# Performance work log

Hardware: AMD Instinct MI355X
Metric: run time of the kernel (lower is better)

## Reference

```python
import jax, jax.numpy as jnp
import numpy as np

N_V = 6890  # SMPL vertices
N_J = 24    # SMPL joints
# standard SMPL kinematic tree: PARENT[i-1] is parent of joint i (i=1..23)
PARENT = np.array([0, 0, 0, 1, 2, 3, 4, 5, 6, 7, 8, 9, 9, 9, 12, 13, 14, 16, 17, 18, 19, 20, 21], dtype=np.int64)


def rodrigues(r):
    """Axis-angle [N,3] -> rotation matrices [N,3,3] (batch Rodrigues)."""
    angle = jnp.sqrt(jnp.sum(r * r, axis=-1, keepdims=True) + 1e-8)  # [N,1]
    axis = r / angle
    c = jnp.cos(angle)[..., None]  # [N,1,1]
    s = jnp.sin(angle)[..., None]
    x, y, z = axis[..., 0], axis[..., 1], axis[..., 2]
    zeros = jnp.zeros_like(x)
    K = jnp.stack([zeros, -z, y, z, zeros, -x, -y, x, zeros], axis=-1).reshape(-1, 3, 3)
    outer = axis[..., :, None] * axis[..., None, :]
    I = jnp.eye(3, dtype=r.dtype)
    return c * I + (1.0 - c) * outer + s * K


def setup_inputs() -> dict:
    key = jax.random.key(0)
    ks = jax.random.split(key, 7)
    B = 1024
    pose = jax.random.normal(ks[0], (B, 72), dtype=jnp.float32) * 0.4
    beta = jax.random.normal(ks[1], (B, 10), dtype=jnp.float32)
    shapedirs = jax.random.normal(ks[2], (N_V, 3, 10), dtype=jnp.float32) * 0.03
    posedirs = jax.random.normal(ks[3], (N_V, 3, 207), dtype=jnp.float32) * 0.01
    v_template = jax.random.normal(ks[4], (N_V, 3), dtype=jnp.float32)
    Jreg = jax.random.uniform(ks[5], (N_J, N_V), dtype=jnp.float32)
    J_regressor = Jreg / jnp.sum(Jreg, axis=1, keepdims=True)  # rows sum to 1 like SMPL
    w = jax.random.uniform(ks[6], (N_V, N_J), dtype=jnp.float32)
    weights = w / jnp.sum(w, axis=1, keepdims=True)  # convex skinning weights
    return {"pose": pose, "beta": beta, "shapedirs": shapedirs, "posedirs": posedirs,
            "v_template": v_template, "J_regressor": J_regressor, "weights": weights}


def reference(pose, beta, shapedirs, posedirs, v_template, J_regressor, weights):
    B = pose.shape[0]
    # shape blend shapes: v_shaped = shapedirs @ beta + template  [B,6890,3]
    v_shaped = jnp.einsum('vcs,bs->bvc', shapedirs, beta) + v_template[None]
    J = jnp.einsum('jv,bvc->bjc', J_regressor, v_shaped)
    # pose -> rotation matrices
    R = rodrigues(pose.reshape(-1, 3)).reshape(B, N_J, 3, 3)
    # pose blend shapes from (R - I) of non-root joints  [B,207]
    lrotmin = (R[:, 1:] - jnp.eye(3, dtype=R.dtype)).reshape(B, 207)
    v_posed = v_shaped + jnp.einsum('vcp,bp->bvc', posedirs, lrotmin)
    # relative joint locations
    J_rel = jnp.concatenate([J[:, :1], J[:, 1:] - J[:, PARENT]], axis=1)  # [B,24,3]
    # local transforms [B,24,4,4]
    G_top = jnp.concatenate([R, J_rel[..., None]], axis=-1)  # [B,24,3,4]
    pad_row = jnp.broadcast_to(jnp.array([0., 0., 0., 1.], dtype=R.dtype), (B, N_J, 1, 4))
    G_local = jnp.concatenate([G_top, pad_row], axis=2)
    # forward kinematics along the chain (fixed 24-joint loop)
    Gs = [G_local[:, 0]]
    for i in range(1, N_J):
        Gs.append(jnp.matmul(Gs[PARENT[i - 1]], G_local[:, i]))
    G = jnp.stack(Gs, axis=1)  # [B,24,4,4]
    # remove rest-pose transform: subtract G @ [J,0] from last column
    J_h = jnp.concatenate([J, jnp.zeros((B, N_J, 1), dtype=J.dtype)], axis=2)  # [B,24,4]
    corr = jnp.einsum('bjmn,bjn->bjm', G, J_h)  # [B,24,4]
    G = G - jnp.pad(corr[..., None], ((0, 0), (0, 0), (0, 0), (3, 0)))
    # skinning: per-vertex transform T = weights @ G  [B,6890,4,4]
    T = jnp.einsum('vj,bjmn->bvmn', weights, G)
    v_h = jnp.concatenate([v_posed, jnp.ones((B, N_V, 1), dtype=v_posed.dtype)], axis=-1)
    v = jnp.einsum('bvmn,bvn->bvm', T, v_h)[..., :3]
    return v
```

## Files before the change

### kernel.cpp

```cpp
#include <hip/hip_runtime.h>
#include <hip/hip_bf16.h>

#define N_V 6890
#define NVPAD 6912
#define N_J 24
#define NREAL 20670
#define NPROWS 27648
#define KDIM 224
#define FB 64
#define FV 64
#define SHP 260
#define NXT 108

typedef __attribute__((ext_vector_type(8))) short bf16x8;
typedef __attribute__((ext_vector_type(4))) float f32x4;

__constant__ int c_par[23] = {0,0,0,1,2,3,4,5,6,7,8,9,9,9,12,13,14,16,17,18,19,20,21};

static __device__ __forceinline__ unsigned short f2bf(float f) {
    unsigned int u = __float_as_uint(f);
    unsigned int r = (u + 0x7fffu + ((u >> 16) & 1u)) >> 16;
    return (unsigned short)r;
}
static __device__ __forceinline__ unsigned int pkbf(float a, float b) {
    return ((__float_as_uint(a) + 0x8000u) >> 16) |
           ((__float_as_uint(b) + 0x8000u) & 0xffff0000u);
}
static __device__ __forceinline__ size_t fragidx(int r, int k) {
    return ((size_t)((r >> 4) * 7 + (k >> 5)) << 9) +
           ((size_t)((r & 15) + (((k >> 3) & 3) << 4)) << 3) + (k & 7);
}

#define WS_PARTIAL 0
#define WS_USHORT  7128
#define U_AMF  0
#define U_BPF  229376
#define U_GBF  6422528
#define U_WBF  6946816

#define JREG_BLOCKS 192
#define BPF_BLOCKS  (NPROWS / 16)
#define WBF_BLOCKS  (NVPAD * 32 / 256)

static __device__ __forceinline__ float bval(const float* pd, const float* sd,
                                             const float* vt, int nc, int k) {
    if (k < 207)  return pd[(size_t)nc * 207 + k];
    if (k < 217)  return sd[(size_t)nc * 10 + (k - 207)];
    if (k == 217) return vt[nc];
    return 0.f;
}

__global__ __launch_bounds__(256)
void k_pre(const float* __restrict__ Jreg,
           const float* __restrict__ shapedirs,
           const float* __restrict__ v_template,
           const float* __restrict__ posedirs,
           const float* __restrict__ weights,
           float* __restrict__ partial,
           unsigned short* __restrict__ Bpf,
           unsigned short* __restrict__ Wbf) {
    const int bid = blockIdx.x;
    const int tid = threadIdx.x;

    if (bid < JREG_BLOCKS) {
        const int j = bid >> 3, chunk = bid & 7;
        const int per = (N_V + 7) / 8;
        const int v0 = chunk * per;
        const int v1 = (v0 + per < N_V) ? (v0 + per) : N_V;
        float acc[33];
#pragma unroll
        for (int k = 0; k < 33; ++k) acc[k] = 0.f;
        for (int v = v0 + tid; v < v1; v += 256) {
            const float w = Jreg[j * N_V + v];
            const float* sd = shapedirs + (size_t)v * 30;
#pragma unroll
            for (int k = 0; k < 30; ++k) acc[k] += w * sd[k];
            acc[30] += w * v_template[v * 3 + 0];
            acc[31] += w * v_template[v * 3 + 1];
            acc[32] += w * v_template[v * 3 + 2];
        }
#pragma unroll
        for (int k = 0; k < 33; ++k) {
            float x = acc[k];
            for (int off = 32; off > 0; off >>= 1) x += __shfl_down(x, off);
            acc[k] = x;
        }
        __shared__ float red[4][33];
        const int wave = tid >> 6, lane = tid & 63;
        if (lane == 0) {
#pragma unroll
            for (int k = 0; k < 33; ++k) red[wave][k] = acc[k];
        }
        __syncthreads();
        if (tid < 33) {
            partial[(j * 8 + chunk) * 33 + tid] =
                red[0][tid] + red[1][tid] + red[2][tid] + red[3][tid];
        }
    } else if (bid < JREG_BLOCKS + BPF_BLOCKS) {
        __shared__ float tile[16][228];
        const int r16 = bid - JREG_BLOCKS;
        {
            const int row = tid >> 4;
            const int k0 = (tid & 15) * 14;
            const int np = r16 * 16 + row;
            const int v = np >> 2, cc = np & 3;
            if (cc < 3 && v < N_V) {
                const int nc = v * 3 + cc;
                const float* pd = posedirs + (size_t)nc * 207;
#pragma unroll
                for (int i = 0; i < 14; ++i) {
                    const int k = k0 + i;
                    float val;
                    if (k < 207)       val = pd[k];
                    else if (k < 217)  val = shapedirs[(size_t)nc * 10 + (k - 207)];
                    else if (k == 217) val = v_template[nc];
                    else               val = 0.f;
                    tile[row][k] = val;
                }
            } else {
#pragma unroll
                for (int i = 0; i < 14; ++i) tile[row][k0 + i] = 0.f;
            }
        }
        __syncthreads();
        const int l = tid >> 2;
        const int row = l & 15;
        const int kblk = (l >> 4) * 8;
        const int e2 = (tid & 3) * 2;
        unsigned short* dst = Bpf + ((size_t)r16 * 7) * 512 + (size_t)tid * 2;
#pragma unroll
        for (int ks = 0; ks < 7; ++ks) {
            const int k = ks * 32 + kblk + e2;
            ushort2 o;
            o.x = f2bf(tile[row][k]);
            o.y = f2bf(tile[row][k + 1]);
            *(ushort2*)(dst + (size_t)ks * 512) = o;
        }
    } else {
        const int idx = (bid - JREG_BLOCKS - BPF_BLOCKS) * 256 + tid;
        const int v = idx >> 5, k = idx & 31;
        float val = (v < N_V && k < 24) ? weights[(size_t)v * 24 + k] : 0.f;
        Wbf[idx] = f2bf(val);
    }
}

__global__ __launch_bounds__(512)
void k_joints(const float* __restrict__ pose, const float* __restrict__ beta,
              const float* __restrict__ partial,
              unsigned short* __restrict__ Amf,
              unsigned short* __restrict__ Gbf) {
    const int tid = threadIdx.x;
    const int wid = tid >> 6;
    const int j = tid & 63;
    const int b = blockIdx.x * 8 + wid;
    __shared__ float sJS[24][30];
    __shared__ float sJt_[24][3];
    __shared__ float sJ[8][24][3];
    __shared__ float sG[8][24][12];

    for (int idx = tid; idx < 792; idx += 512) {
        const int jj = idx / 33, kk = idx - jj * 33;
        float s = 0.f;
#pragma unroll
        for (int c = 0; c < 8; ++c) s += partial[(jj * 8 + c) * 33 + kk];
        if (kk < 30) sJS[jj][kk] = s;
        else         sJt_[jj][kk - 30] = s;
    }

    for (int idx = j; idx < 224; idx += 64) {
        int mn, jj;
        if (idx < 128) { mn = 12 + (idx >> 5); jj = idx & 31; }
        else { const int q = idx - 128; mn = q >> 3; jj = 24 + (q & 7); }
        Gbf[(size_t)b * 512 + mn * 32 + jj] = 0;
    }
    __syncthreads();

    float R[9];
    if (j < 24) {
        const float* bt = beta + b * 10;
#pragma unroll
        for (int c = 0; c < 3; ++c) {
            float s = sJt_[j][c];
#pragma unroll
            for (int t = 0; t < 10; ++t) s += sJS[j][c * 10 + t] * bt[t];
            sJ[wid][j][c] = s;
        }
        const float rx = pose[b * 72 + 3 * j + 0];
        const float ry = pose[b * 72 + 3 * j + 1];
        const float rz = pose[b * 72 + 3 * j + 2];
        const float ang = sqrtf(rx * rx + ry * ry + rz * rz + 1e-8f);
        const float inv = 1.f / ang;
        const float x = rx * inv, y = ry * inv, z = rz * inv;
        const float c = cosf(ang), s = sinf(ang);
        const float ic = 1.f - c;
        R[0] = c + ic * x * x;     R[1] = ic * x * y - s * z; R[2] = ic * x * z + s * y;
        R[3] = ic * x * y + s * z; R[4] = c + ic * y * y;     R[5] = ic * y * z - s * x;
        R[6] = ic * x * z - s * y; R[7] = ic * y * z + s * x; R[8] = c + ic * z * z;
        if (j >= 1) {
            const int kb = (j - 1) * 9;
#pragma unroll
            for (int k = 0; k < 9; ++k)
                Amf[fragidx(b & 15, kb + k) + (size_t)(b >> 4) * 3584] =
                    f2bf(R[k] - ((k == 0 || k == 4 || k == 8) ? 1.f : 0.f));
        }
    } else if (j < 41) {
        const int k = 207 + (j - 24);
        float val = (k < 217) ? beta[b * 10 + (k - 207)] : (k == 217 ? 1.f : 0.f);
        Amf[fragidx(b & 15, k) + (size_t)(b >> 4) * 3584] = f2bf(val);
    }
    __syncthreads();
    if (j < 24) {
        float t0, t1, t2;
        if (j == 0) { t0 = sJ[wid][0][0]; t1 = sJ[wid][0][1]; t2 = sJ[wid][0][2]; }
        else {
            const int p = c_par[j - 1];
            t0 = sJ[wid][j][0] - sJ[wid][p][0];
            t1 = sJ[wid][j][1] - sJ[wid][p][1];
            t2 = sJ[wid][j][2] - sJ[wid][p][2];
        }
        sG[wid][j][0] = R[0]; sG[wid][j][1] = R[1]; sG[wid][j][2]  = R[2]; sG[wid][j][3]  = t0;
        sG[wid][j][4] = R[3]; sG[wid][j][5] = R[4]; sG[wid][j][6]  = R[5]; sG[wid][j][7]  = t1;
        sG[wid][j][8] = R[6]; sG[wid][j][9] = R[7]; sG[wid][j][10] = R[8]; sG[wid][j][11] = t2;
    }
    __syncthreads();
    if (j == 0) {
        for (int i = 1; i < 24; ++i) {
            const int p = c_par[i - 1];
            float P[12], L[12];
#pragma unroll
            for (int k = 0; k < 12; ++k) { P[k] = sG[wid][p][k]; L[k] = sG[wid][i][k]; }
#pragma unroll
            for (int m = 0; m < 3; ++m) {
#pragma unroll
                for (int n = 0; n < 3; ++n)
                    sG[wid][i][m * 4 + n] = P[m * 4] * L[n] + P[m * 4 + 1] * L[4 + n] + P[m * 4 + 2] * L[8 + n];
                sG[wid][i][m * 4 + 3] = P[m * 4] * L[3] + P[m * 4 + 1] * L[7] + P[m * 4 + 2] * L[11] + P[m * 4 + 3];
            }
        }
    }
    __syncthreads();
    if (j < 24) {
        const float jx = sJ[wid][j][0], jy = sJ[wid][j][1], jz = sJ[wid][j][2];
#pragma unroll
        for (int m = 0; m < 3; ++m) {
            const float corr = sG[wid][j][m * 4] * jx + sG[wid][j][m * 4 + 1] * jy + sG[wid][j][m * 4 + 2] * jz;
            Gbf[(size_t)b * 512 + (m * 4 + 0) * 32 + j] = f2bf(sG[wid][j][m * 4 + 0]);
            Gbf[(size_t)b * 512 + (m * 4 + 1) * 32 + j] = f2bf(sG[wid][j][m * 4 + 1]);
            Gbf[(size_t)b * 512 + (m * 4 + 2) * 32 + j] = f2bf(sG[wid][j][m * 4 + 2]);
            Gbf[(size_t)b * 512 + (m * 4 + 3) * 32 + j] = f2bf(sG[wid][j][m * 4 + 3] - corr);
        }
    }
}

__global__ __launch_bounds__(512, 4)
void k_fused(const unsigned short* __restrict__ Amf,
             const unsigned short* __restrict__ Bpf,
             const unsigned short* __restrict__ Gbf,
             const unsigned short* __restrict__ Wbf,
             float* __restrict__ out) {
    __shared__ unsigned short sH[FB * SHP];
    const int tid = threadIdx.x;
    const int wid = tid >> 6, l = tid & 63;
    const int c16 = l & 15, p = l >> 4;

    const int wg = ((blockIdx.x & 7) * 216) + (blockIdx.x >> 3);
    const int xt = wg >> 4;
    const int bg = wg & 15;
    const int v0 = xt * FV;
    const int b0 = bg * FB;

    bf16x8 bw[4];
#pragma unroll
    for (int g = 0; g < 4; ++g)
        bw[g] = *(const bf16x8*)&Wbf[(size_t)(v0 + g * 16 + c16) * 32 + p * 8];
    const int bwv = wid * 8;
    const unsigned short* gG = Gbf + (size_t)(b0 + bwv) * 512 + c16 * 32 + p * 8;

    f32x4 acc[2][4];
#pragma unroll
    for (int i = 0; i < 2; ++i)
#pragma unroll
        for (int j = 0; j < 4; ++j) acc[i][j] = (f32x4){0.f, 0.f, 0.f, 0.f};

    const unsigned short* pbf = Bpf + ((size_t)(xt * 16 + wid * 2) * 7) * 512 + (size_t)l * 8;
    const unsigned short* pam = Amf + ((size_t)(bg * 4) * 7) * 512 + (size_t)l * 8;

#pragma unroll
    for (int ks = 0; ks < 7; ++ks) {
        bf16x8 af[2], bfr[4];
#pragma unroll
        for (int mi = 0; mi < 2; ++mi)
            af[mi] = *(const bf16x8*)(pbf + (size_t)(mi * 7 + ks) * 512);
#pragma unroll
        for (int bj = 0; bj < 4; ++bj)
            bfr[bj] = *(const bf16x8*)(pam + (size_t)(bj * 7 + ks) * 512);
        __builtin_amdgcn_s_setprio(1);
#pragma unroll
        for (int mi = 0; mi < 2; ++mi)
#pragma unroll
            for (int bj = 0; bj < 4; ++bj)
                acc[mi][bj] = __builtin_amdgcn_mfma_f32_16x16x32_bf16(af[mi], bfr[bj], acc[mi][bj], 0, 0, 0);
        __builtin_amdgcn_s_setprio(0);
    }

    bf16x8 agA[4], agB[4];
#pragma unroll
    for (int j = 0; j < 4; ++j)
        agA[j] = *(const bf16x8*)(gG + (size_t)j * 512);

    {
        const int vbase = wid * 8 + p;
#pragma unroll
        for (int mi = 0; mi < 2; ++mi) {
#pragma unroll
            for (int bj = 0; bj < 4; ++bj) {
                const int vl = vbase + mi * 4;
                const int bl = bj * 16 + c16;
                uint2 u;
                u.x = pkbf(acc[mi][bj][0], acc[mi][bj][1]);
                u.y = pkbf(acc[mi][bj][2], acc[mi][bj][3]);
                *(uint2*)&sH[bl * SHP + vl * 4] = u;
            }
        }
    }
    __syncthreads();

#pragma unroll
    for (int j = 0; j < 4; ++j)
        agB[j] = *(const bf16x8*)(gG + (size_t)(4 + j) * 512);

    bool st[4];
#pragma unroll
    for (int g = 0; g < 4; ++g)
        st[g] = (v0 + g * 16 + c16 < N_V) && (p < 3);
    float* ob = out + (size_t)(b0 + bwv) * NREAL + (size_t)(v0 + c16) * 3 + p;
    const unsigned short* sh = &sH[bwv * SHP + c16 * 4];

    __builtin_amdgcn_s_setprio(1);
#pragma unroll
    for (int j = 0; j < 4; ++j) {
#pragma unroll
        for (int g = 0; g < 4; ++g) {
            const f32x4 t = __builtin_amdgcn_mfma_f32_16x16x32_bf16(agA[j], bw[g], (f32x4){0.f,0.f,0.f,0.f}, 0, 0, 0);
            const uint2 h = *(const uint2*)(sh + j * SHP + g * 64);
            const float x = __uint_as_float(h.x << 16);
            const float y = __uint_as_float(h.x & 0xffff0000u);
            const float z = __uint_as_float(h.y << 16);
            const float r = t[0] * x + t[1] * y + t[2] * z + t[3];
            if (st[g]) ob[(size_t)j * NREAL + g * 48] = r;
        }
    }
    __builtin_amdgcn_s_setprio(0);
#pragma unroll
    for (int j = 0; j < 4; ++j) {
#pragma unroll
        for (int g = 0; g < 4; ++g) {
            const f32x4 t = __builtin_amdgcn_mfma_f32_16x16x32_bf16(agB[j], bw[g], (f32x4){0.f,0.f,0.f,0.f}, 0, 0, 0);
            const uint2 h = *(const uint2*)(sh + (4 + j) * SHP + g * 64);
            const float x = __uint_as_float(h.x << 16);
            const float y = __uint_as_float(h.x & 0xffff0000u);
            const float z = __uint_as_float(h.y << 16);
            const float r = t[0] * x + t[1] * y + t[2] * z + t[3];
            if (st[g]) ob[(size_t)(4 + j) * NREAL + g * 48] = r;
        }
    }
}

extern "C" void kernel_launch(void* const* d_in, const int* in_sizes, int n_in,
                              void* d_out, int out_size, void* d_ws, size_t ws_size,
                              hipStream_t stream) {
    const float* pose       = (const float*)d_in[0];
    const float* beta       = (const float*)d_in[1];
    const float* shapedirs  = (const float*)d_in[2];
    const float* posedirs   = (const float*)d_in[3];
    const float* v_template = (const float*)d_in[4];
    const float* Jreg       = (const float*)d_in[5];
    const float* weights    = (const float*)d_in[6];
    float* out = (float*)d_out;

    const int B = in_sizes[0] / 72;

    float* ws = (float*)d_ws;
    float* partial = ws + WS_PARTIAL;
    unsigned short* ubase = (unsigned short*)(ws + WS_USHORT);
    unsigned short* Amf = ubase + U_AMF;
    unsigned short* Bpf = ubase + U_BPF;
    unsigned short* Gbf = ubase + U_GBF;
    unsigned short* Wbf = ubase + U_WBF;

    k_pre<<<JREG_BLOCKS + BPF_BLOCKS + WBF_BLOCKS, 256, 0, stream>>>(
        Jreg, shapedirs, v_template, posedirs, weights, partial, Bpf, Wbf);
    k_joints<<<B / 8, 512, 0, stream>>>(pose, beta, partial, Amf, Gbf);
    k_fused<<<NXT * (B / FB), 512, 0, stream>>>(Amf, Bpf, Gbf, Wbf, out);
}
```

Baseline: 73.09 us.

## Reschedule prep stages so joint kinematics overlaps posedirs and weights conversion

The joint-regressor reduction now runs alone in a small first kernel. The per-batch joint and forward-kinematics work moves out of its own launch into a second kernel, which also handles the posedirs and weights bf16 repacking as separate block ranges. The joint stage now uses 4 batches per 256-thread block, so it can run concurrently with the repacking instead of waiting behind it. This keeps the launch count at three and is meant to shorten the serial critical path before the fused GEMM kernel. The trade-off is that the jreg kernel, at 192 blocks, now runs alone without other work to fill the device.

```diff
diff --git a/kernel.cpp b/kernel.cpp
--- a/kernel.cpp
+++ b/kernel.cpp
@@ -39,66 +39,170 @@
 #define U_WBF  6946816
 
 #define JREG_BLOCKS 192
+#define JNT_BLOCKS  256
 #define BPF_BLOCKS  (NPROWS / 16)
 #define WBF_BLOCKS  (NVPAD * 32 / 256)
 
-static __device__ __forceinline__ float bval(const float* pd, const float* sd,
-                                             const float* vt, int nc, int k) {
-    if (k < 207)  return pd[(size_t)nc * 207 + k];
-    if (k < 217)  return sd[(size_t)nc * 10 + (k - 207)];
-    if (k == 217) return vt[nc];
-    return 0.f;
-}
-
 __global__ __launch_bounds__(256)
-void k_pre(const float* __restrict__ Jreg,
+void k_jreg(const float* __restrict__ Jreg,
+            const float* __restrict__ shapedirs,
+            const float* __restrict__ v_template,
+            float* __restrict__ partial) {
+    const int bid = blockIdx.x;
+    const int tid = threadIdx.x;
+    const int j = bid >> 3, chunk = bid & 7;
+    const int per = (N_V + 7) / 8;
+    const int v0 = chunk * per;
+    const int v1 = (v0 + per < N_V) ? (v0 + per) : N_V;
+    float acc[33];
+#pragma unroll
+    for (int k = 0; k < 33; ++k) acc[k] = 0.f;
+    for (int v = v0 + tid; v < v1; v += 256) {
+        const float w = Jreg[j * N_V + v];
+        const float* sd = shapedirs + (size_t)v * 30;
+#pragma unroll
+        for (int k = 0; k < 30; ++k) acc[k] += w * sd[k];
+        acc[30] += w * v_template[v * 3 + 0];
+        acc[31] += w * v_template[v * 3 + 1];
+        acc[32] += w * v_template[v * 3 + 2];
+    }
+#pragma unroll
+    for (int k = 0; k < 33; ++k) {
+        float x = acc[k];
+        for (int off = 32; off > 0; off >>= 1) x += __shfl_down(x, off);
+        acc[k] = x;
+    }
+    __shared__ float red[4][33];
+    const int wave = tid >> 6, lane = tid & 63;
+    if (lane == 0) {
+#pragma unroll
+        for (int k = 0; k < 33; ++k) red[wave][k] = acc[k];
+    }
+    __syncthreads();
+    if (tid < 33) {
+        partial[(j * 8 + chunk) * 33 + tid] =
+            red[0][tid] + red[1][tid] + red[2][tid] + red[3][tid];
+    }
+}
+
+__global__ __launch_bounds__(256)
+void k_mid(const float* __restrict__ pose, const float* __restrict__ beta,
+           const float* __restrict__ partial,
            const float* __restrict__ shapedirs,
            const float* __restrict__ v_template,
            const float* __restrict__ posedirs,
            const float* __restrict__ weights,
-           float* __restrict__ partial,
+           unsigned short* __restrict__ Amf,
+           unsigned short* __restrict__ Gbf,
            unsigned short* __restrict__ Bpf,
            unsigned short* __restrict__ Wbf) {
     const int bid = blockIdx.x;
     const int tid = threadIdx.x;
 
-    if (bid < JREG_BLOCKS) {
-        const int j = bid >> 3, chunk = bid & 7;
-        const int per = (N_V + 7) / 8;
-        const int v0 = chunk * per;
-        const int v1 = (v0 + per < N_V) ? (v0 + per) : N_V;
-        float acc[33];
-#pragma unroll
-        for (int k = 0; k < 33; ++k) acc[k] = 0.f;
-        for (int v = v0 + tid; v < v1; v += 256) {
-            const float w = Jreg[j * N_V + v];
-            const float* sd = shapedirs + (size_t)v * 30;
-#pragma unroll
-            for (int k = 0; k < 30; ++k) acc[k] += w * sd[k];
-            acc[30] += w * v_template[v * 3 + 0];
-            acc[31] += w * v_template[v * 3 + 1];
-            acc[32] += w * v_template[v * 3 + 2];
-        }
-#pragma unroll
-        for (int k = 0; k < 33; ++k) {
-            float x = acc[k];
-            for (int off = 32; off > 0; off >>= 1) x += __shfl_down(x, off);
-            acc[k] = x;
-        }
-        __shared__ float red[4][33];
-        const int wave = tid >> 6, lane = tid & 63;
-        if (lane == 0) {
-#pragma unroll
-            for (int k = 0; k < 33; ++k) red[wave][k] = acc[k];
-        }
-        __syncthreads();
-        if (tid < 33) {
-            partial[(j * 8 + chunk) * 33 + tid] =
-                red[0][tid] + red[1][tid] + red[2][tid] + red[3][tid];
-        }
-    } else if (bid < JREG_BLOCKS + BPF_BLOCKS) {
+    if (bid < JNT_BLOCKS) {
+        const int wid = tid >> 6;
+        const int j = tid & 63;
+        const int b = bid * 4 + wid;
+        __shared__ float sJS[24][30];
+        __shared__ float sJt_[24][3];
+        __shared__ float sJ[4][24][3];
+        __shared__ float sG[4][24][12];
+
+        for (int idx = tid; idx < 792; idx += 256) {
+            const int jj = idx / 33, kk = idx - jj * 33;
+            float s = 0.f;
+#pragma unroll
+            for (int c = 0; c < 8; ++c) s += partial[(jj * 8 + c) * 33 + kk];
+            if (kk < 30) sJS[jj][kk] = s;
+            else         sJt_[jj][kk - 30] = s;
+        }
+
+        for (int idx = j; idx < 224; idx += 64) {
+            int mn, jj;
+            if (idx < 128) { mn = 12 + (idx >> 5); jj = idx & 31; }
+            else { const int q = idx - 128; mn = q >> 3; jj = 24 + (q & 7); }
+            Gbf[(size_t)b * 512 + mn * 32 + jj] = 0;
+        }
+        __syncthreads();
+
+        float R[9];
+        if (j < 24) {
+            const float* bt = beta + b * 10;
+#pragma unroll
+            for (int c = 0; c < 3; ++c) {
+                float s = sJt_[j][c];
+#pragma unroll
+                for (int t = 0; t < 10; ++t) s += sJS[j][c * 10 + t] * bt[t];
+                sJ[wid][j][c] = s;
+            }
+            const float rx = pose[b * 72 + 3 * j + 0];
+            const float ry = pose[b * 72 + 3 * j + 1];
+            const float rz = pose[b * 72 + 3 * j + 2];
+            const float ang = sqrtf(rx * rx + ry * ry + rz * rz + 1e-8f);
+            const float inv = 1.f / ang;
+            const float x = rx * inv, y = ry * inv, z = rz * inv;
+            const float c = cosf(ang), s = sinf(ang);
+            const float ic = 1.f - c;
+            R[0] = c + ic * x * x;     R[1] = ic * x * y - s * z; R[2] = ic * x * z + s * y;
+            R[3] = ic * x * y + s * z; R[4] = c + ic * y * y;     R[5] = ic * y * z - s * x;
+            R[6] = ic * x * z - s * y; R[7] = ic * y * z + s * x; R[8] = c + ic * z * z;
+            if (j >= 1) {
+                const int kb = (j - 1) * 9;
+#pragma unroll
+                for (int k = 0; k < 9; ++k)
+                    Amf[fragidx(b & 15, kb + k) + (size_t)(b >> 4) * 3584] =
+                        f2bf(R[k] - ((k == 0 || k == 4 || k == 8) ? 1.f : 0.f));
+            }
+        } else if (j < 41) {
+            const int k = 207 + (j - 24);
+            float val = (k < 217) ? beta[b * 10 + (k - 207)] : (k == 217 ? 1.f : 0.f);
+            Amf[fragidx(b & 15, k) + (size_t)(b >> 4) * 3584] = f2bf(val);
+        }
+        __syncthreads();
+        if (j < 24) {
+            float t0, t1, t2;
+            if (j == 0) { t0 = sJ[wid][0][0]; t1 = sJ[wid][0][1]; t2 = sJ[wid][0][2]; }
+            else {
+                const int p = c_par[j - 1];
+                t0 = sJ[wid][j][0] - sJ[wid][p][0];
+                t1 = sJ[wid][j][1] - sJ[wid][p][1];
+                t2 = sJ[wid][j][2] - sJ[wid][p][2];
+            }
+            sG[wid][j][0] = R[0]; sG[wid][j][1] = R[1]; sG[wid][j][2]  = R[2]; sG[wid][j][3]  = t0;
+            sG[wid][j][4] = R[3]; sG[wid][j][5] = R[4]; sG[wid][j][6]  = R[5]; sG[wid][j][7]  = t1;
+            sG[wid][j][8] = R[6]; sG[wid][j][9] = R[7]; sG[wid][j][10] = R[8]; sG[wid][j][11] = t2;
+        }
+        __syncthreads();
+        if (j == 0) {
+            for (int i = 1; i < 24; ++i) {
+                const int p = c_par[i - 1];
+                float P[12], L[12];
+#pragma unroll
+                for (int k = 0; k < 12; ++k) { P[k] = sG[wid][p][k]; L[k] = sG[wid][i][k]; }
+#pragma unroll
+                for (int m = 0; m < 3; ++m) {
+#pragma unroll
+                    for (int n = 0; n < 3; ++n)
+                        sG[wid][i][m * 4 + n] = P[m * 4] * L[n] + P[m * 4 + 1] * L[4 + n] + P[m * 4 + 2] * L[8 + n];
+                    sG[wid][i][m * 4 + 3] = P[m * 4] * L[3] + P[m * 4 + 1] * L[7] + P[m * 4 + 2] * L[11] + P[m * 4 + 3];
+                }
+            }
+        }
+        __syncthreads();
+        if (j < 24) {
+            const float jx = sJ[wid][j][0], jy = sJ[wid][j][1], jz = sJ[wid][j][2];
+#pragma unroll
+            for (int m = 0; m < 3; ++m) {
+                const float corr = sG[wid][j][m * 4] * jx + sG[wid][j][m * 4 + 1] * jy + sG[wid][j][m * 4 + 2] * jz;
+                Gbf[(size_t)b * 512 + (m * 4 + 0) * 32 + j] = f2bf(sG[wid][j][m * 4 + 0]);
+                Gbf[(size_t)b * 512 + (m * 4 + 1) * 32 + j] = f2bf(sG[wid][j][m * 4 + 1]);
+                Gbf[(size_t)b * 512 + (m * 4 + 2) * 32 + j] = f2bf(sG[wid][j][m * 4 + 2]);
+                Gbf[(size_t)b * 512 + (m * 4 + 3) * 32 + j] = f2bf(sG[wid][j][m * 4 + 3] - corr);
+            }
+        }
+    } else if (bid < JNT_BLOCKS + BPF_BLOCKS) {
         __shared__ float tile[16][228];
-        const int r16 = bid - JREG_BLOCKS;
+        const int r16 = bid - JNT_BLOCKS;
         {
             const int row = tid >> 4;
             const int k0 = (tid & 15) * 14;
@@ -137,118 +241,10 @@
             *(ushort2*)(dst + (size_t)ks * 512) = o;
         }
     } else {
-        const int idx = (bid - JREG_BLOCKS - BPF_BLOCKS) * 256 + tid;
+        const int idx = (bid - JNT_BLOCKS - BPF_BLOCKS) * 256 + tid;
         const int v = idx >> 5, k = idx & 31;
         float val = (v < N_V && k < 24) ? weights[(size_t)v * 24 + k] : 0.f;
         Wbf[idx] = f2bf(val);
-    }
-}
-
-__global__ __launch_bounds__(512)
-void k_joints(const float* __restrict__ pose, const float* __restrict__ beta,
-              const float* __restrict__ partial,
-              unsigned short* __restrict__ Amf,
-              unsigned short* __restrict__ Gbf) {
-    const int tid = threadIdx.x;
-    const int wid = tid >> 6;
-    const int j = tid & 63;
-    const int b = blockIdx.x * 8 + wid;
-    __shared__ float sJS[24][30];
-    __shared__ float sJt_[24][3];
-    __shared__ float sJ[8][24][3];
-    __shared__ float sG[8][24][12];
-
-    for (int idx = tid; idx < 792; idx += 512) {
-        const int jj = idx / 33, kk = idx - jj * 33;
-        float s = 0.f;
-#pragma unroll
-        for (int c = 0; c < 8; ++c) s += partial[(jj * 8 + c) * 33 + kk];
-        if (kk < 30) sJS[jj][kk] = s;
-        else         sJt_[jj][kk - 30] = s;
-    }
-
-    for (int idx = j; idx < 224; idx += 64) {
-        int mn, jj;
-        if (idx < 128) { mn = 12 + (idx >> 5); jj = idx & 31; }
-        else { const int q = idx - 128; mn = q >> 3; jj = 24 + (q & 7); }
-        Gbf[(size_t)b * 512 + mn * 32 + jj] = 0;
-    }
-    __syncthreads();
-
-    float R[9];
-    if (j < 24) {
-        const float* bt = beta + b * 10;
-#pragma unroll
-        for (int c = 0; c < 3; ++c) {
-            float s = sJt_[j][c];
-#pragma unroll
-            for (int t = 0; t < 10; ++t) s += sJS[j][c * 10 + t] * bt[t];
-            sJ[wid][j][c] = s;
-        }
-        const float rx = pose[b * 72 + 3 * j + 0];
-        const float ry = pose[b * 72 + 3 * j + 1];
-        const float rz = pose[b * 72 + 3 * j + 2];
-        const float ang = sqrtf(rx * rx + ry * ry + rz * rz + 1e-8f);
-        const float inv = 1.f / ang;
-        const float x = rx * inv, y = ry * inv, z = rz * inv;
-        const float c = cosf(ang), s = sinf(ang);
-        const float ic = 1.f - c;
-        R[0] = c + ic * x * x;     R[1] = ic * x * y - s * z; R[2] = ic * x * z + s * y;
-        R[3] = ic * x * y + s * z; R[4] = c + ic * y * y;     R[5] = ic * y * z - s * x;
-        R[6] = ic * x * z - s * y; R[7] = ic * y * z + s * x; R[8] = c + ic * z * z;
-        if (j >= 1) {
-            const int kb = (j - 1) * 9;
-#pragma unroll
-            for (int k = 0; k < 9; ++k)
-                Amf[fragidx(b & 15, kb + k) + (size_t)(b >> 4) * 3584] =
-                    f2bf(R[k] - ((k == 0 || k == 4 || k == 8) ? 1.f : 0.f));
-        }
-    } else if (j < 41) {
-        const int k = 207 + (j - 24);
-        float val = (k < 217) ? beta[b * 10 + (k - 207)] : (k == 217 ? 1.f : 0.f);
-        Amf[fragidx(b & 15, k) + (size_t)(b >> 4) * 3584] = f2bf(val);
-    }
-    __syncthreads();
-    if (j < 24) {
-        float t0, t1, t2;
-        if (j == 0) { t0 = sJ[wid][0][0]; t1 = sJ[wid][0][1]; t2 = sJ[wid][0][2]; }
-        else {
-            const int p = c_par[j - 1];
-            t0 = sJ[wid][j][0] - sJ[wid][p][0];
-            t1 = sJ[wid][j][1] - sJ[wid][p][1];
-            t2 = sJ[wid][j][2] - sJ[wid][p][2];
-        }
-        sG[wid][j][0] = R[0]; sG[wid][j][1] = R[1]; sG[wid][j][2]  = R[2]; sG[wid][j][3]  = t0;
-        sG[wid][j][4] = R[3]; sG[wid][j][5] = R[4]; sG[wid][j][6]  = R[5]; sG[wid][j][7]  = t1;
-        sG[wid][j][8] = R[6]; sG[wid][j][9] = R[7]; sG[wid][j][10] = R[8]; sG[wid][j][11] = t2;
-    }
-    __syncthreads();
-    if (j == 0) {
-        for (int i = 1; i < 24; ++i) {
-            const int p = c_par[i - 1];
-            float P[12], L[12];
-#pragma unroll
-            for (int k = 0; k < 12; ++k) { P[k] = sG[wid][p][k]; L[k] = sG[wid][i][k]; }
-#pragma unroll
-            for (int m = 0; m < 3; ++m) {
-#pragma unroll
-                for (int n = 0; n < 3; ++n)
-                    sG[wid][i][m * 4 + n] = P[m * 4] * L[n] + P[m * 4 + 1] * L[4 + n] + P[m * 4 + 2] * L[8 + n];
-                sG[wid][i][m * 4 + 3] = P[m * 4] * L[3] + P[m * 4 + 1] * L[7] + P[m * 4 + 2] * L[11] + P[m * 4 + 3];
-            }
-        }
-    }
-    __syncthreads();
-    if (j < 24) {
-        const float jx = sJ[wid][j][0], jy = sJ[wid][j][1], jz = sJ[wid][j][2];
-#pragma unroll
-        for (int m = 0; m < 3; ++m) {
-            const float corr = sG[wid][j][m * 4] * jx + sG[wid][j][m * 4 + 1] * jy + sG[wid][j][m * 4 + 2] * jz;
-            Gbf[(size_t)b * 512 + (m * 4 + 0) * 32 + j] = f2bf(sG[wid][j][m * 4 + 0]);
-            Gbf[(size_t)b * 512 + (m * 4 + 1) * 32 + j] = f2bf(sG[wid][j][m * 4 + 1]);
-            Gbf[(size_t)b * 512 + (m * 4 + 2) * 32 + j] = f2bf(sG[wid][j][m * 4 + 2]);
-            Gbf[(size_t)b * 512 + (m * 4 + 3) * 32 + j] = f2bf(sG[wid][j][m * 4 + 3] - corr);
-        }
     }
 }
 
@@ -388,8 +384,9 @@
     unsigned short* Gbf = ubase + U_GBF;
     unsigned short* Wbf = ubase + U_WBF;
 
-    k_pre<<<JREG_BLOCKS + BPF_BLOCKS + WBF_BLOCKS, 256, 0, stream>>>(
-        Jreg, shapedirs, v_template, posedirs, weights, partial, Bpf, Wbf);
-    k_joints<<<B / 8, 512, 0, stream>>>(pose, beta, partial, Amf, Gbf);
+    k_jreg<<<JREG_BLOCKS, 256, 0, stream>>>(Jreg, shapedirs, v_template, partial);
+    k_mid<<<JNT_BLOCKS + BPF_BLOCKS + WBF_BLOCKS, 256, 0, stream>>>(
+        pose, beta, partial, shapedirs, v_template, posedirs, weights,
+        Amf, Gbf, Bpf, Wbf);
     k_fused<<<NXT * (B / FB), 512, 0, stream>>>(Amf, Bpf, Gbf, Wbf, out);
 }
```

Result: faster. 69.27 us, median of 2 (-5.2%).
